# Optimization experiments

Hardware: AMD Instinct MI355X
Metric: run time of the kernel (lower is better)

## Reference

```python
import jax, jax.numpy as jnp
import numpy as np

B, C, N, OUT, K = 8, 64, 4096, 64, 16


def setup_inputs() -> dict:
    key = jax.random.key(0)
    k0, k1, k2, k3, k4 = jax.random.split(key, 5)
    x = jax.random.normal(k0, (B, C, N, 1), jnp.float32)
    s1 = 1.0 / np.sqrt(2 * C)
    s2 = 1.0 / np.sqrt(OUT)
    W1 = jax.random.uniform(k1, (2 * C, OUT), jnp.float32, -s1, s1)
    b1 = jax.random.uniform(k2, (OUT,), jnp.float32, -s1, s1)
    W2 = jax.random.uniform(k3, (OUT, OUT), jnp.float32, -s2, s2)
    b2 = jax.random.uniform(k4, (OUT,), jnp.float32, -s2, s2)
    return {"x": x, "W1": W1, "b1": b1, "W2": W2, "b2": b2}


def reference(x, W1, b1, W2, b2):
    # x: [B, C, N, 1] -> node features [B, N, C]
    xb = x[..., 0].transpose(0, 2, 1)  # [B, N, C]
    # kNN per batch element (PyG knn includes the point itself)
    sq = jnp.sum(xb * xb, axis=-1)  # [B, N]
    d2 = sq[:, :, None] + sq[:, None, :] - 2.0 * jnp.einsum('bnc,bmc->bnm', xb, xb)
    _, idx = jax.lax.top_k(-d2, K)  # [B, N, K] neighbor indices
    # gather neighbor features: [B, N, K, C]
    xj = jax.vmap(lambda f, i: jnp.take(f, i, axis=0))(xb, idx)
    xi = xb[:, :, None, :]  # [B, N, 1, C]
    # EdgeConv edge features: [x_i, x_j - x_i]
    e = jnp.concatenate([jnp.broadcast_to(xi, xj.shape), xj - xi], axis=-1)  # [B,N,K,2C]
    h = jax.nn.relu(e @ W1 + b1)
    h = jax.nn.relu(h @ W2 + b2)
    out = jnp.max(h, axis=2)  # max aggregation over neighbors -> [B, N, OUT]
    return out.transpose(0, 2, 1)[..., None]  # [B, OUT, N, 1]
```

## Files before the change

### kernel.cpp

```cpp
#include <hip/hip_runtime.h>
#include <stdint.h>

#define BB 8
#define CCH 64
#define NPB 4096
#define NPTS (BB*NPB)
#define PPW 8

typedef float  f32x2  __attribute__((ext_vector_type(2)));
typedef float  f32x4v __attribute__((ext_vector_type(4)));
typedef short  bf16x8 __attribute__((ext_vector_type(8)));
typedef unsigned short u16x8 __attribute__((ext_vector_type(8)));
typedef unsigned long long u64;
typedef unsigned int u32;

__device__ __forceinline__ unsigned short f2bf(float x) {
    u32 u = __float_as_uint(x);
    u += 0x7FFFu + ((u >> 16) & 1u);
    return (unsigned short)(u >> 16);
}

template<typename T>
__device__ __forceinline__ void sort16(T* key) {
#pragma unroll
    for (int kk = 2; kk <= 16; kk <<= 1) {
#pragma unroll
        for (int j = kk >> 1; j > 0; j >>= 1) {
#pragma unroll
            for (int i = 0; i < 16; ++i) {
                int l = i ^ j;
                if (l > i) {
                    bool up = ((i & kk) == 0);
                    T a = key[i], c = key[l];
                    bool cond = up ? (c < a) : (a < c);
                    key[i] = cond ? c : a;
                    key[l] = cond ? a : c;
                }
            }
        }
    }
}

template<typename T>
__device__ __forceinline__ void merge16(T* list, const T* key) {
    T m[16];
#pragma unroll
    for (int i = 0; i < 16; ++i) {
        T a = list[i], c = key[15 - i];
        m[i] = (c < a) ? c : a;
    }
#pragma unroll
    for (int j = 8; j > 0; j >>= 1) {
#pragma unroll
        for (int i = 0; i < 16; ++i) {
            if ((i & j) == 0) {
                T a = m[i], c = m[i + j];
                bool cond = c < a;
                m[i]     = cond ? c : a;
                m[i + j] = cond ? a : c;
            }
        }
    }
#pragma unroll
    for (int i = 0; i < 16; ++i) list[i] = m[i];
}

__global__ void k_transpose(const float* __restrict__ x, float* __restrict__ xb) {
    __shared__ float tile[64][65];
    int b  = blockIdx.y;
    int n0 = blockIdx.x * 64;
    int tx = threadIdx.x, ty = threadIdx.y;
    const float* xp = x + (size_t)b * CCH * NPB;
#pragma unroll
    for (int r = 0; r < 8; ++r) {
        int c = ty + r * 8;
        tile[c][tx] = xp[(size_t)c * NPB + n0 + tx];
    }
    __syncthreads();
    float* xbp = xb + ((size_t)b * NPB + n0) * CCH;
#pragma unroll
    for (int r = 0; r < 8; ++r) {
        int nn = ty + r * 8;
        xbp[(size_t)nn * CCH + tx] = tile[tx][nn];
    }
}

__global__ void k_sq(const float* __restrict__ xb, float* __restrict__ sq) {
    int p = blockIdx.x * 256 + threadIdx.x;
    const float4* r = (const float4*)(xb + (size_t)p * CCH);
    float s = 0.0f;
#pragma unroll
    for (int i = 0; i < 16; ++i) {
        float4 v = r[i];
        s += v.x * v.x + v.y * v.y + v.z * v.z + v.w * v.w;
    }
    sq[p] = s;
}

__global__ void k_cast(const float* __restrict__ xb, unsigned short* __restrict__ xh) {
    int i = blockIdx.x * 256 + threadIdx.x;
    const float4* s = (const float4*)(xb + (size_t)i * 8);
    float4 v0 = s[0], v1 = s[1];
    u16x8 o;
    o[0] = f2bf(v0.x); o[1] = f2bf(v0.y); o[2] = f2bf(v0.z); o[3] = f2bf(v0.w);
    o[4] = f2bf(v1.x); o[5] = f2bf(v1.y); o[6] = f2bf(v1.z); o[7] = f2bf(v1.w);
    *(u16x8*)(xh + (size_t)i * 8) = o;
}

__global__ void k_prepw(const float* __restrict__ W1, const float* __restrict__ W2,
                        unsigned short* __restrict__ W1t, unsigned short* __restrict__ W2t) {
    int t = blockIdx.x * 256 + threadIdx.x;
    if (t < 8192) {
        int o = t >> 7, k = t & 127;
        float v = (k < 64) ? (W1[k * 64 + o] - W1[(64 + k) * 64 + o]) : W1[k * 64 + o];
        W1t[o * 128 + k] = f2bf(v);
    } else if (t < 12288) {
        int u = t - 8192;
        int o = u >> 6, j = u & 63;
        W2t[o * 64 + j] = f2bf(W2[j * 64 + o]);
    }
}

__global__ __launch_bounds__(256) void k_gemm(const unsigned short* __restrict__ xh,
                                              const float* __restrict__ sq,
                                              u32* __restrict__ cand) {
    __shared__ float dtile[64][65];
    __shared__ u32 llist[64][65];
    int b = blockIdx.y >> 6;
    const unsigned short* xhB = xh + (size_t)b * NPB * CCH;
    const float* sqB = sq + (size_t)b * NPB;
    u32* candB = cand + (size_t)b * 64 * NPB * 16;
    int l = threadIdx.x & 63;
    int w = threadIdx.x >> 6;
    int m0 = (blockIdx.y & 63) * 64;
    int n0 = blockIdx.x * 64;
    const unsigned short* ap = xhB + (size_t)(m0 + w * 16 + (l & 15)) * CCH + ((l >> 4) * 8);
    bf16x8 a0 = *(const bf16x8*)ap;
    bf16x8 a1 = *(const bf16x8*)(ap + 32);
    f32x4v z = {0.f, 0.f, 0.f, 0.f};
    f32x4v acc[4];
#pragma unroll
    for (int cg = 0; cg < 4; ++cg) {
        const unsigned short* bp = xhB + (size_t)(n0 + cg * 16 + (l & 15)) * CCH + ((l >> 4) * 8);
        bf16x8 b0 = *(const bf16x8*)bp;
        bf16x8 b1 = *(const bf16x8*)(bp + 32);
        acc[cg] = __builtin_amdgcn_mfma_f32_16x16x32_bf16(a0, b0, z, 0, 0, 0);
        acc[cg] = __builtin_amdgcn_mfma_f32_16x16x32_bf16(a1, b1, acc[cg], 0, 0, 0);
    }
    int rb = m0 + w * 16 + (l >> 4) * 4;
    float4 sr = *(const float4*)(sqB + rb);
    float sqr[4] = {sr.x, sr.y, sr.z, sr.w};
#pragma unroll
    for (int cg = 0; cg < 4; ++cg) {
        int cit = cg * 16 + (l & 15);
        float sc = sqB[n0 + cit];
#pragma unroll
        for (int j = 0; j < 4; ++j) {
            float v = fmaxf(fmaf(-2.f, acc[cg][j], sqr[j] + sc), 0.f);
            dtile[w * 16 + (l >> 4) * 4 + j][cit] = v;
        }
    }
    __syncthreads();
    {
        int row = l, ch = w;
        u32 key[16];
#pragma unroll
        for (int e = 0; e < 16; ++e) {
            float v = dtile[row][ch * 16 + e];
            key[e] = ((u32)f2bf(v) << 16) | (u32)(n0 + ch * 16 + e);
        }
        sort16(key);
#pragma unroll
        for (int i = 0; i < 16; ++i) llist[row][ch * 16 + i] = key[i];
    }
    __syncthreads();
    if (threadIdx.x < 64) {
        int r2 = threadIdx.x;
        u32 list[16], tmp[16];
#pragma unroll
        for (int i = 0; i < 16; ++i) list[i] = llist[r2][i];
#pragma unroll
        for (int ch2 = 1; ch2 < 4; ++ch2) {
#pragma unroll
            for (int i = 0; i < 16; ++i) tmp[i] = llist[r2][ch2 * 16 + i];
            merge16(list, tmp);
        }
        u32* cp = candB + ((size_t)blockIdx.x * NPB + (m0 + r2)) * 16;
#pragma unroll
        for (int i = 0; i < 16; ++i) cp[i] = list[i];
    }
}

__global__ __launch_bounds__(256, 1) void k_post(const u32* __restrict__ cand,
                                                 const float* __restrict__ xb,
                                                 const float* __restrict__ sq,
                                                 int* __restrict__ idxo) {
    int l  = threadIdx.x & 63;
    int rl = __builtin_amdgcn_readfirstlane(threadIdx.x >> 6);
    int rowg = blockIdx.x * 4 + rl;
    int b    = rowg >> 12;
    int row  = rowg & 4095;
    const float* xbB = xb + ((size_t)b << 12) * CCH;
    const float* sqB = sq + ((size_t)b << 12);
    const u32* candB = cand + (size_t)b * 64 * NPB * 16;
    const float* xr = xbB + (size_t)row * CCH;
    float rr[64];
#pragma unroll
    for (int i = 0; i < 16; ++i) {
        float4 v = *(const float4*)(xr + i * 4);
        rr[4*i] = v.x; rr[4*i+1] = v.y; rr[4*i+2] = v.z; rr[4*i+3] = v.w;
    }
    u32 karr[16];
    {
        const uint4* cp = (const uint4*)(candB + ((size_t)l * NPB + row) * 16);
#pragma unroll
        for (int i = 0; i < 4; ++i) {
            uint4 v = cp[i];
            karr[4*i] = v.x; karr[4*i+1] = v.y; karr[4*i+2] = v.z; karr[4*i+3] = v.w;
        }
    }
    u32 cur = karr[0];
    int ci = 0;
    u32 mycol = 0xFFFFFFFFu;
#pragma unroll
    for (int r = 0; r < 48; ++r) {
        u32 mv = cur;
#pragma unroll
        for (int o = 32; o > 0; o >>= 1) {
            u32 t = __shfl_xor(mv, o);
            mv = t < mv ? t : mv;
        }
        if (l == r) mycol = mv;
        if (cur == mv) {
            ci++;
            u32 nxt = 0xFFFFFFFFu;
#pragma unroll
            for (int q = 15; q >= 1; --q) nxt = (ci == q) ? karr[q] : nxt;
            cur = nxt;
        }
    }
    u64 mykey = ~0ULL;
    if (mycol != 0xFFFFFFFFu) {
        int col = (int)(mycol & 0xFFFFu);
        const float* xj = xbB + (size_t)col * CCH;
        float lo = 0.f, hi = 0.f;
#pragma unroll
        for (int q = 0; q < 8; ++q) {
            float4 v  = *(const float4*)(xj + q * 4);
            float4 wv = *(const float4*)(xj + 32 + q * 4);
            lo = fmaf(v.x,  rr[4*q+0], lo);
            lo = fmaf(v.y,  rr[4*q+1], lo);
            lo = fmaf(v.z,  rr[4*q+2], lo);
            lo = fmaf(v.w,  rr[4*q+3], lo);
            hi = fmaf(wv.x, rr[32+4*q+0], hi);
            hi = fmaf(wv.y, rr[32+4*q+1], hi);
            hi = fmaf(wv.z, rr[32+4*q+2], hi);
            hi = fmaf(wv.w, rr[32+4*q+3], hi);
        }
        float d = fmaf(-2.f, lo + hi, sqB[col]);
        u32 fb = __float_as_uint(d);
        fb ^= (fb >> 31) ? 0xFFFFFFFFu : 0x80000000u;
        mykey = ((u64)fb << 32) | (u32)col;
    }
    u64 curk = mykey;
#pragma unroll
    for (int r = 0; r < 16; ++r) {
        u64 mv = curk;
#pragma unroll
        for (int o = 32; o > 0; o >>= 1) {
            u64 t = (u64)__shfl_xor((long long)mv, o);
            mv = t < mv ? t : mv;
        }
        if (curk == mv) curk = ~0ULL;
        if (l == 0) idxo[(size_t)rowg * 16 + r] = (int)(mv & 0xFFFFFFFFu);
    }
}

__global__ __launch_bounds__(256, 1) void k_mlp2(const unsigned short* __restrict__ xh,
                                                 const int* __restrict__ idx,
                                                 const unsigned short* __restrict__ W1t,
                                                 const unsigned short* __restrict__ W2t,
                                                 const float* __restrict__ b1,
                                                 const float* __restrict__ b2,
                                                 float* __restrict__ out) {
    __shared__ unsigned short h1l[4][16 * 72];
    int l   = threadIdx.x & 63;
    int wib = threadIdx.x >> 6;
    int e   = l & 15;
    int kg  = l >> 4;
    int wave = blockIdx.x * 4 + wib;
    unsigned short* hl = h1l[wib];

    bf16x8 w1f[4][4];
#pragma unroll
    for (int nt = 0; nt < 4; ++nt)
#pragma unroll
        for (int s = 0; s < 4; ++s)
            w1f[nt][s] = *(const bf16x8*)(W1t + (size_t)(nt * 16 + e) * 128 + s * 32 + kg * 8);
    bf16x8 w2f[4][2];
#pragma unroll
    for (int nt = 0; nt < 4; ++nt)
#pragma unroll
        for (int s = 0; s < 2; ++s)
            w2f[nt][s] = *(const bf16x8*)(W2t + (size_t)(nt * 16 + e) * 64 + s * 32 + kg * 8);
    float b1v[4], b2v[4];
#pragma unroll
    for (int nt = 0; nt < 4; ++nt) { b1v[nt] = b1[nt * 16 + e]; b2v[nt] = b2[nt * 16 + e]; }

    int p0 = wave * PPW;
    int bb = p0 >> 12;
    int n0 = p0 & 4095;
    const unsigned short* xhB = xh + ((size_t)bb << 12) * CCH;
    f32x4v z = {0.f, 0.f, 0.f, 0.f};
    float mx[4][PPW];
#pragma unroll
    for (int nt = 0; nt < 4; ++nt)
#pragma unroll
        for (int pi = 0; pi < PPW; ++pi) mx[nt][pi] = 0.f;

#pragma unroll
    for (int pi = 0; pi < PPW; ++pi) {
        int n = n0 + pi;
        int je = idx[((size_t)(p0 + pi)) * 16 + e];
        bf16x8 a[4];
        a[0] = *(const bf16x8*)(xhB + (size_t)n * 64 + kg * 8);
        a[1] = *(const bf16x8*)(xhB + (size_t)n * 64 + 32 + kg * 8);
        a[2] = *(const bf16x8*)(xhB + (size_t)je * 64 + kg * 8);
        a[3] = *(const bf16x8*)(xhB + (size_t)je * 64 + 32 + kg * 8);
#pragma unroll
        for (int nt = 0; nt < 4; ++nt) {
            f32x4v acc = z;
#pragma unroll
            for (int s = 0; s < 4; ++s)
                acc = __builtin_amdgcn_mfma_f32_16x16x32_bf16(a[s], w1f[nt][s], acc, 0, 0, 0);
#pragma unroll
            for (int j = 0; j < 4; ++j) {
                float h = fmaxf(acc[j] + b1v[nt], 0.f);
                hl[(kg * 4 + j) * 72 + nt * 16 + e] = f2bf(h);
            }
        }
        bf16x8 a2[2];
        a2[0] = *(const bf16x8*)(hl + (size_t)e * 72 + kg * 8);
        a2[1] = *(const bf16x8*)(hl + (size_t)e * 72 + 32 + kg * 8);
#pragma unroll
        for (int nt = 0; nt < 4; ++nt) {
            f32x4v acc = z;
            acc = __builtin_amdgcn_mfma_f32_16x16x32_bf16(a2[0], w2f[nt][0], acc, 0, 0, 0);
            acc = __builtin_amdgcn_mfma_f32_16x16x32_bf16(a2[1], w2f[nt][1], acc, 0, 0, 0);
            float m4 = 0.f;
#pragma unroll
            for (int j = 0; j < 4; ++j)
                m4 = fmaxf(m4, fmaxf(acc[j] + b2v[nt], 0.f));
            mx[nt][pi] = m4;
        }
    }
#pragma unroll
    for (int nt = 0; nt < 4; ++nt)
#pragma unroll
        for (int pi = 0; pi < PPW; ++pi) {
            float v = mx[nt][pi];
            v = fmaxf(v, __shfl_xor(v, 16));
            v = fmaxf(v, __shfl_xor(v, 32));
            mx[nt][pi] = v;
        }
    if (kg == 0) {
#pragma unroll
        for (int nt = 0; nt < 4; ++nt) {
            float* op = out + ((size_t)bb * 64 + nt * 16 + e) * NPB + n0;
#pragma unroll
            for (int pi = 0; pi < PPW; ++pi) op[pi] = mx[nt][pi];
        }
    }
}

extern "C" void kernel_launch(void* const* d_in, const int* in_sizes, int n_in,
                              void* d_out, int out_size, void* d_ws, size_t ws_size,
                              hipStream_t stream) {
    const float* x  = (const float*)d_in[0];
    const float* W1 = (const float*)d_in[1];
    const float* b1 = (const float*)d_in[2];
    const float* W2 = (const float*)d_in[3];
    const float* b2 = (const float*)d_in[4];
    float* out = (float*)d_out;

    const size_t MB = 1024 * 1024;
    char* ws = (char*)d_ws;
    float*          xb  = (float*)(ws);
    unsigned short* xh  = (unsigned short*)(ws + 8 * MB);
    float*          sq  = (float*)(ws + 12 * MB);
    unsigned short* W1t = (unsigned short*)(ws + 12 * MB + 256 * 1024);
    unsigned short* W2t = (unsigned short*)(ws + 12 * MB + 272 * 1024);
    u32*            cand = (u32*)(ws + 13 * MB);
    size_t candAll = (size_t)BB * 64 * NPB * 16 * 4;
    size_t needF = 13 * MB + candAll + (size_t)NPTS * 16 * 4;

    hipLaunchKernelGGL(k_transpose, dim3(NPB / 64, BB), dim3(64, 8), 0, stream, x, xb);
    hipLaunchKernelGGL(k_sq, dim3(NPTS / 256), dim3(256), 0, stream, xb, sq);
    hipLaunchKernelGGL(k_cast, dim3(NPTS * CCH / 8 / 256), dim3(256), 0, stream, xb, xh);
    hipLaunchKernelGGL(k_prepw, dim3(48), dim3(256), 0, stream, W1, W2, W1t, W2t);

    if (ws_size >= needF + MB) {
        int* idxb = (int*)(ws + 13 * MB + candAll);
        hipLaunchKernelGGL(k_gemm, dim3(NPB / 64, 64 * BB), dim3(256), 0, stream,
                           xh, sq, cand);
        hipLaunchKernelGGL(k_post, dim3(NPTS / 4), dim3(256), 0, stream,
                           cand, xb, sq, idxb);
        hipLaunchKernelGGL(k_mlp2, dim3(NPTS / PPW / 4), dim3(256), 0, stream,
                           xh, idxb, W1t, W2t, b1, b2, out);
    } else {
        int* idxb = (int*)(ws + 30 * MB);
        for (int b = 0; b < BB; ++b) {
            const unsigned short* xhB = xh + (size_t)b * NPB * CCH;
            const float* xbB = xb + (size_t)b * NPB * CCH;
            const float* sqB = sq + (size_t)b * NPB;
            hipLaunchKernelGGL(k_gemm, dim3(NPB / 64, 64), dim3(256), 0, stream,
                               xhB, sqB, cand);
            hipLaunchKernelGGL(k_post, dim3(NPB / 4), dim3(256), 0, stream,
                               cand, xbB, sqB, idxb + (size_t)b * NPB * 16);
        }
        hipLaunchKernelGGL(k_mlp2, dim3(NPTS / PPW / 4), dim3(256), 0, stream,
                           xh, idxb, W1t, W2t, b1, b2, out);
    }
}
```

Before: 400.1 us.

## Fuse prep kernels into transpose and replace serial candidate selection with threshold search

Folds the squared-norm and bf16-cast kernels into the transpose kernel, using a wave shuffle reduction for the norm, which removes two launches and two re-reads of xb. In k_post, the 48-round serial shuffle-min selection of candidates is replaced by a 16-step binary search on the 16-bit approximate distance key to find a threshold. Candidates at or below the threshold are then compacted into LDS slots by prefix sum, and the final top-16 is taken with a full bitonic sort across the wave instead of 16 min-reduction rounds. Ties at the threshold may admit more or fewer than 48 candidates, since the compaction truncates at 64 slots, so the selected set can differ slightly from the old one.

Measured after the change: 322.6 us. 1.24x faster.

```diff
diff --git a/kernel.cpp b/kernel.cpp
--- a/kernel.cpp
+++ b/kernel.cpp
@@ -65,7 +65,8 @@
     for (int i = 0; i < 16; ++i) list[i] = m[i];
 }
 
-__global__ void k_transpose(const float* __restrict__ x, float* __restrict__ xb) {
+__global__ void k_transpose(const float* __restrict__ x, float* __restrict__ xb,
+                            unsigned short* __restrict__ xh, float* __restrict__ sq) {
     __shared__ float tile[64][65];
     int b  = blockIdx.y;
     int n0 = blockIdx.x * 64;
@@ -78,33 +79,19 @@
     }
     __syncthreads();
     float* xbp = xb + ((size_t)b * NPB + n0) * CCH;
+    unsigned short* xhp = xh + ((size_t)b * NPB + n0) * CCH;
+    float* sqp = sq + (size_t)b * NPB + n0;
 #pragma unroll
     for (int r = 0; r < 8; ++r) {
         int nn = ty + r * 8;
-        xbp[(size_t)nn * CCH + tx] = tile[tx][nn];
-    }
-}
-
-__global__ void k_sq(const float* __restrict__ xb, float* __restrict__ sq) {
-    int p = blockIdx.x * 256 + threadIdx.x;
-    const float4* r = (const float4*)(xb + (size_t)p * CCH);
-    float s = 0.0f;
-#pragma unroll
-    for (int i = 0; i < 16; ++i) {
-        float4 v = r[i];
-        s += v.x * v.x + v.y * v.y + v.z * v.z + v.w * v.w;
-    }
-    sq[p] = s;
-}
-
-__global__ void k_cast(const float* __restrict__ xb, unsigned short* __restrict__ xh) {
-    int i = blockIdx.x * 256 + threadIdx.x;
-    const float4* s = (const float4*)(xb + (size_t)i * 8);
-    float4 v0 = s[0], v1 = s[1];
-    u16x8 o;
-    o[0] = f2bf(v0.x); o[1] = f2bf(v0.y); o[2] = f2bf(v0.z); o[3] = f2bf(v0.w);
-    o[4] = f2bf(v1.x); o[5] = f2bf(v1.y); o[6] = f2bf(v1.z); o[7] = f2bf(v1.w);
-    *(u16x8*)(xh + (size_t)i * 8) = o;
+        float v = tile[tx][nn];
+        xbp[(size_t)nn * CCH + tx] = v;
+        xhp[(size_t)nn * CCH + tx] = f2bf(v);
+        float s = v * v;
+#pragma unroll
+        for (int o = 32; o > 0; o >>= 1) s += __shfl_xor(s, o);
+        if (tx == 0) sqp[nn] = s;
+    }
 }
 
 __global__ void k_prepw(const float* __restrict__ W1, const float* __restrict__ W2,
@@ -195,6 +182,7 @@
                                                  const float* __restrict__ xb,
                                                  const float* __restrict__ sq,
                                                  int* __restrict__ idxo) {
+    __shared__ u32 slots[4][64];
     int l  = threadIdx.x & 63;
     int rl = __builtin_amdgcn_readfirstlane(threadIdx.x >> 6);
     int rowg = blockIdx.x * 4 + rl;
@@ -219,61 +207,74 @@
             karr[4*i] = v.x; karr[4*i+1] = v.y; karr[4*i+2] = v.z; karr[4*i+3] = v.w;
         }
     }
-    u32 cur = karr[0];
-    int ci = 0;
-    u32 mycol = 0xFFFFFFFFu;
-#pragma unroll
-    for (int r = 0; r < 48; ++r) {
-        u32 mv = cur;
-#pragma unroll
-        for (int o = 32; o > 0; o >>= 1) {
-            u32 t = __shfl_xor(mv, o);
-            mv = t < mv ? t : mv;
-        }
-        if (l == r) mycol = mv;
-        if (cur == mv) {
-            ci++;
-            u32 nxt = 0xFFFFFFFFu;
-#pragma unroll
-            for (int q = 15; q >= 1; --q) nxt = (ci == q) ? karr[q] : nxt;
-            cur = nxt;
-        }
-    }
-    u64 mykey = ~0ULL;
-    if (mycol != 0xFFFFFFFFu) {
-        int col = (int)(mycol & 0xFFFFu);
+    u32 lo = 0, hi = 0xFFFFu;
+#pragma unroll
+    for (int it = 0; it < 16; ++it) {
+        u32 mid = (lo + hi) >> 1;
+        int c = 0;
+#pragma unroll
+        for (int i = 0; i < 16; ++i) c += ((karr[i] >> 16) <= mid) ? 1 : 0;
+#pragma unroll
+        for (int o = 32; o > 0; o >>= 1) c += __shfl_xor(c, o);
+        bool ge = (c >= 48);
+        lo = ge ? lo : (mid + 1);
+        hi = ge ? mid : hi;
+    }
+    u32 vstar = hi;
+    int cnt = 0;
+#pragma unroll
+    for (int i = 0; i < 16; ++i) cnt += ((karr[i] >> 16) <= vstar) ? 1 : 0;
+    int pre = cnt;
+#pragma unroll
+    for (int d = 1; d < 64; d <<= 1) {
+        int t = __shfl_up(pre, d);
+        if (l >= d) pre += t;
+    }
+    int base = pre - cnt;
+    u32* sl = slots[rl];
+    sl[l] = 0xFFFFFFFFu;
+#pragma unroll
+    for (int i = 0; i < 16; ++i) {
+        if (i < cnt) {
+            int s = base + i;
+            if (s < 64) sl[s] = karr[i];
+        }
+    }
+    u32 mk = sl[l];
+    u64 key = ~0ULL;
+    if (mk != 0xFFFFFFFFu) {
+        int col = (int)(mk & 0xFFFFu);
         const float* xj = xbB + (size_t)col * CCH;
-        float lo = 0.f, hi = 0.f;
+        float lod = 0.f, hid = 0.f;
 #pragma unroll
         for (int q = 0; q < 8; ++q) {
             float4 v  = *(const float4*)(xj + q * 4);
             float4 wv = *(const float4*)(xj + 32 + q * 4);
-            lo = fmaf(v.x,  rr[4*q+0], lo);
-            lo = fmaf(v.y,  rr[4*q+1], lo);
-            lo = fmaf(v.z,  rr[4*q+2], lo);
-            lo = fmaf(v.w,  rr[4*q+3], lo);
-            hi = fmaf(wv.x, rr[32+4*q+0], hi);
-            hi = fmaf(wv.y, rr[32+4*q+1], hi);
-            hi = fmaf(wv.z, rr[32+4*q+2], hi);
-            hi = fmaf(wv.w, rr[32+4*q+3], hi);
-        }
-        float d = fmaf(-2.f, lo + hi, sqB[col]);
+            lod = fmaf(v.x,  rr[4*q+0], lod);
+            lod = fmaf(v.y,  rr[4*q+1], lod);
+            lod = fmaf(v.z,  rr[4*q+2], lod);
+            lod = fmaf(v.w,  rr[4*q+3], lod);
+            hid = fmaf(wv.x, rr[32+4*q+0], hid);
+            hid = fmaf(wv.y, rr[32+4*q+1], hid);
+            hid = fmaf(wv.z, rr[32+4*q+2], hid);
+            hid = fmaf(wv.w, rr[32+4*q+3], hid);
+        }
+        float d = fmaf(-2.f, lod + hid, sqB[col]);
         u32 fb = __float_as_uint(d);
         fb ^= (fb >> 31) ? 0xFFFFFFFFu : 0x80000000u;
-        mykey = ((u64)fb << 32) | (u32)col;
-    }
-    u64 curk = mykey;
-#pragma unroll
-    for (int r = 0; r < 16; ++r) {
-        u64 mv = curk;
-#pragma unroll
-        for (int o = 32; o > 0; o >>= 1) {
-            u64 t = (u64)__shfl_xor((long long)mv, o);
-            mv = t < mv ? t : mv;
-        }
-        if (curk == mv) curk = ~0ULL;
-        if (l == 0) idxo[(size_t)rowg * 16 + r] = (int)(mv & 0xFFFFFFFFu);
-    }
+        key = ((u64)fb << 32) | (u32)col;
+    }
+#pragma unroll
+    for (int kk = 2; kk <= 64; kk <<= 1) {
+#pragma unroll
+        for (int j = kk >> 1; j > 0; j >>= 1) {
+            u64 p = (u64)__shfl_xor((long long)key, j);
+            bool keep_min = (((l & kk) == 0) == ((l & j) == 0));
+            bool plt = p < key;
+            key = keep_min ? (plt ? p : key) : (plt ? key : p);
+        }
+    }
+    if (l < 16) idxo[(size_t)rowg * 16 + l] = (int)(key & 0xFFFFFFFFu);
 }
 
 __global__ __launch_bounds__(256, 1) void k_mlp2(const unsigned short* __restrict__ xh,
@@ -394,9 +395,7 @@
     size_t candAll = (size_t)BB * 64 * NPB * 16 * 4;
     size_t needF = 13 * MB + candAll + (size_t)NPTS * 16 * 4;
 
-    hipLaunchKernelGGL(k_transpose, dim3(NPB / 64, BB), dim3(64, 8), 0, stream, x, xb);
-    hipLaunchKernelGGL(k_sq, dim3(NPTS / 256), dim3(256), 0, stream, xb, sq);
-    hipLaunchKernelGGL(k_cast, dim3(NPTS * CCH / 8 / 256), dim3(256), 0, stream, xb, xh);
+    hipLaunchKernelGGL(k_transpose, dim3(NPB / 64, BB), dim3(64, 8), 0, stream, x, xb, xh, sq);
     hipLaunchKernelGGL(k_prepw, dim3(48), dim3(256), 0, stream, W1, W2, W1t, W2t);
 
     if (ws_size >= needF + MB) {
```
